# Optimization experiments

Measured on AMD Instinct MI355X. Metric: run time of the kernel, lower is better.

The kernel has to match this reference:

```python
import jax, jax.numpy as jnp
import numpy as np

NTAPS = 63
BATCH = 32
SAMPLES = 2_097_152


def setup_inputs() -> dict:
    key = jax.random.key(0)
    k1, k2, k3, k4 = jax.random.split(key, 4)
    x = jax.random.normal(k1, (BATCH, 1, SAMPLES), dtype=jnp.float32)
    b = jax.random.normal(k2, (BATCH, NTAPS), dtype=jnp.float32)
    # adaptor: torch.nn.Linear(63, 63) -> weight (out,in), bias (out,)
    W = jax.random.normal(k3, (NTAPS, NTAPS), dtype=jnp.float32) * (1.0 / np.sqrt(NTAPS))
    bias = jax.random.normal(k4, (NTAPS,), dtype=jnp.float32) * (1.0 / np.sqrt(NTAPS))
    return {"x": x, "b": b, "W": W, "bias": bias}


def reference(x, b, W, bias):
    # x: (bs, 1, s); b: (bs, ntaps)
    bs, ch, s = x.shape
    # adaptor: Linear on filter coefficients
    b = b @ W.T + bias                      # (bs, ntaps)
    ntaps = b.shape[-1]
    pad = ntaps // 2
    # same-length FIR (torch conv1d = cross-correlation)
    xp = jnp.pad(x, ((0, 0), (0, 0), (pad, pad)))   # (bs, 1, s + 2*pad)
    # batched per-sample filters via grouped conv: batch dim -> channel groups
    lhs = xp.reshape(1, bs * ch, -1)        # N=1, C=bs
    rhs = b.reshape(bs, 1, ntaps)           # O=bs, I=1, taps
    y = jax.lax.conv_general_dilated(
        lhs, rhs,
        window_strides=(1,),
        padding="VALID",
        dimension_numbers=("NCH", "OIH", "NCH"),
        feature_group_count=bs,
    )                                       # (1, bs, s)
    return y.reshape(bs, ch, s)
```

## Files before the change

kernel.cpp:

```cpp
#include <hip/hip_runtime.h>

#define NTAPS   63
#define NBATCH  32
#define SAMPLES 2097152
#define ROUT    16
#define BLOCK   256
#define CHUNK   (ROUT * BLOCK)
#define TILE_F  (CHUNK + 64)
#define TILE_B  (TILE_F / 4)
#define PSLOT(o) ((o) + ((o) >> 2))
#define LDS_B   (PSLOT(TILE_B - 1) + 1)

__global__ void filt_kernel(const float* __restrict__ b,
                            const float* __restrict__ W,
                            const float* __restrict__ bias,
                            float* __restrict__ filt) {
    const int batch = blockIdx.x;
    const int t = threadIdx.x;
    if (t < NTAPS) {
        const float* br = b + batch * NTAPS;
        const float* wr = W + t * NTAPS;
        float s = bias[t];
#pragma unroll
        for (int k = 0; k < NTAPS; ++k) s = fmaf(br[k], wr[k], s);
        filt[batch * NTAPS + t] = s;
    }
}

__global__ __launch_bounds__(BLOCK) void fir_kernel(const float* __restrict__ x,
                                                    const float* __restrict__ filt,
                                                    float* __restrict__ y) {
    __shared__ float4 tile[LDS_B];

    const int tid = threadIdx.x;
    const int batch = blockIdx.y;
    const int chunk0 = blockIdx.x * CHUNK;
    const float* __restrict__ xb = x + (size_t)batch * SAMPLES;
    float*       __restrict__ yb = y + (size_t)batch * SAMPLES;
    const float* __restrict__ bf = filt + batch * NTAPS;

    const bool interior = (blockIdx.x != 0) && (blockIdx.x != gridDim.x - 1);
    if (interior) {
#pragma unroll
        for (int r = 0; r < 4; ++r) {
            const int o = r * BLOCK + tid;
            const float4 v = *reinterpret_cast<const float4*>(xb + chunk0 - 32 + 4 * o);
            tile[PSLOT(o)] = v;
        }
        if (tid < TILE_B - 4 * BLOCK) {
            const int o = 4 * BLOCK + tid;
            const float4 v = *reinterpret_cast<const float4*>(xb + chunk0 - 32 + 4 * o);
            tile[PSLOT(o)] = v;
        }
    } else {
#pragma unroll
        for (int r = 0; r < 5; ++r) {
            const int o = r * BLOCK + tid;
            if (o < TILE_B) {
                const int gi = chunk0 - 32 + 4 * o;
                float4 v;
                v.x = (gi + 0 >= 0 && gi + 0 < SAMPLES) ? xb[gi + 0] : 0.0f;
                v.y = (gi + 1 >= 0 && gi + 1 < SAMPLES) ? xb[gi + 1] : 0.0f;
                v.z = (gi + 2 >= 0 && gi + 2 < SAMPLES) ? xb[gi + 2] : 0.0f;
                v.w = (gi + 3 >= 0 && gi + 3 < SAMPLES) ? xb[gi + 3] : 0.0f;
                tile[PSLOT(o)] = v;
            }
        }
    }
    __syncthreads();

    float w[80];
#pragma unroll
    for (int j = 0; j < 20; ++j) {
        const float4 v = tile[5 * tid + j + (j >> 2)];
        w[4 * j + 0] = v.x;
        w[4 * j + 1] = v.y;
        w[4 * j + 2] = v.z;
        w[4 * j + 3] = v.w;
    }

    float acc[ROUT];
#pragma unroll
    for (int r = 0; r < ROUT; ++r) acc[r] = 0.0f;

#pragma unroll
    for (int t = 0; t < NTAPS; ++t) {
        const float c = bf[t];
#pragma unroll
        for (int r = 0; r < ROUT; ++r) acc[r] = fmaf(c, w[r + t + 1], acc[r]);
    }

    const int s0 = chunk0 + tid * ROUT;
#pragma unroll
    for (int j = 0; j < ROUT / 4; ++j) {
        float4 v;
        v.x = acc[4 * j + 0];
        v.y = acc[4 * j + 1];
        v.z = acc[4 * j + 2];
        v.w = acc[4 * j + 3];
        *reinterpret_cast<float4*>(yb + s0 + 4 * j) = v;
    }
}

extern "C" void kernel_launch(void* const* d_in, const int* in_sizes, int n_in,
                              void* d_out, int out_size, void* d_ws, size_t ws_size,
                              hipStream_t stream) {
    const float* x    = (const float*)d_in[0];
    const float* b    = (const float*)d_in[1];
    const float* W    = (const float*)d_in[2];
    const float* bias = (const float*)d_in[3];
    float* y = (float*)d_out;
    float* filt = (float*)d_ws;

    filt_kernel<<<dim3(NBATCH), dim3(64), 0, stream>>>(b, W, bias, filt);

    dim3 grid(SAMPLES / CHUNK, NBATCH);
    fir_kernel<<<grid, dim3(BLOCK), 0, stream>>>(x, filt, y);
}
```

Baseline: 448.8 us.

## Make FIR blocks persistent over chunks with double-buffered LDS and register prefetch

Each block now processes eight consecutive chunks instead of one. The next chunk's input is prefetched into registers while the current chunk is computed, and is staged into a second LDS buffer between iterations. The goal is to hide global load latency behind the FMA work and to amortise block launch and filter-coefficient loads. In exchange, LDS use doubles and register pressure rises, which may lower occupancy, and the grid shrinks by a factor of eight.

```diff
diff --git a/kernel.cpp b/kernel.cpp
--- a/kernel.cpp
+++ b/kernel.cpp
@@ -6,10 +6,14 @@
 #define ROUT    16
 #define BLOCK   256
 #define CHUNK   (ROUT * BLOCK)
+#define NCHUNKS (SAMPLES / CHUNK)
+#define ITERS   8
+#define NBLKX   (NCHUNKS / ITERS)
 #define TILE_F  (CHUNK + 64)
 #define TILE_B  (TILE_F / 4)
 #define PSLOT(o) ((o) + ((o) >> 2))
 #define LDS_B   (PSLOT(TILE_B - 1) + 1)
+#define TAIL_B  (TILE_B - 4 * BLOCK)
 
 __global__ void filt_kernel(const float* __restrict__ b,
                             const float* __restrict__ W,
@@ -30,75 +34,99 @@
 __global__ __launch_bounds__(BLOCK) void fir_kernel(const float* __restrict__ x,
                                                     const float* __restrict__ filt,
                                                     float* __restrict__ y) {
-    __shared__ float4 tile[LDS_B];
+    __shared__ float4 tileA[LDS_B];
+    __shared__ float4 tileB[LDS_B];
 
-    const int tid = threadIdx.x;
+    const int tid   = threadIdx.x;
     const int batch = blockIdx.y;
-    const int chunk0 = blockIdx.x * CHUNK;
+    const int c0    = blockIdx.x * ITERS;
     const float* __restrict__ xb = x + (size_t)batch * SAMPLES;
     float*       __restrict__ yb = y + (size_t)batch * SAMPLES;
     const float* __restrict__ bf = filt + batch * NTAPS;
 
-    const bool interior = (blockIdx.x != 0) && (blockIdx.x != gridDim.x - 1);
-    if (interior) {
+    float4 p0, p1, p2, p3, p4;
+
+    auto load_tile = [&](int c) {
+        const int base = c * CHUNK - 32;
+        if (c != 0 && c != NCHUNKS - 1) {
+            p0 = *reinterpret_cast<const float4*>(xb + base + 4 * (0 * BLOCK + tid));
+            p1 = *reinterpret_cast<const float4*>(xb + base + 4 * (1 * BLOCK + tid));
+            p2 = *reinterpret_cast<const float4*>(xb + base + 4 * (2 * BLOCK + tid));
+            p3 = *reinterpret_cast<const float4*>(xb + base + 4 * (3 * BLOCK + tid));
+            if (tid < TAIL_B)
+                p4 = *reinterpret_cast<const float4*>(xb + base + 4 * (4 * BLOCK + tid));
+        } else {
+            float4* pr[5] = {&p0, &p1, &p2, &p3, &p4};
 #pragma unroll
-        for (int r = 0; r < 4; ++r) {
-            const int o = r * BLOCK + tid;
-            const float4 v = *reinterpret_cast<const float4*>(xb + chunk0 - 32 + 4 * o);
-            tile[PSLOT(o)] = v;
-        }
-        if (tid < TILE_B - 4 * BLOCK) {
-            const int o = 4 * BLOCK + tid;
-            const float4 v = *reinterpret_cast<const float4*>(xb + chunk0 - 32 + 4 * o);
-            tile[PSLOT(o)] = v;
-        }
-    } else {
-#pragma unroll
-        for (int r = 0; r < 5; ++r) {
-            const int o = r * BLOCK + tid;
-            if (o < TILE_B) {
-                const int gi = chunk0 - 32 + 4 * o;
-                float4 v;
-                v.x = (gi + 0 >= 0 && gi + 0 < SAMPLES) ? xb[gi + 0] : 0.0f;
-                v.y = (gi + 1 >= 0 && gi + 1 < SAMPLES) ? xb[gi + 1] : 0.0f;
-                v.z = (gi + 2 >= 0 && gi + 2 < SAMPLES) ? xb[gi + 2] : 0.0f;
-                v.w = (gi + 3 >= 0 && gi + 3 < SAMPLES) ? xb[gi + 3] : 0.0f;
-                tile[PSLOT(o)] = v;
+            for (int r = 0; r < 5; ++r) {
+                const int o = r * BLOCK + tid;
+                if (o < TILE_B) {
+                    const int gi = base + 4 * o;
+                    float4 v;
+                    v.x = (gi + 0 >= 0 && gi + 0 < SAMPLES) ? xb[gi + 0] : 0.0f;
+                    v.y = (gi + 1 >= 0 && gi + 1 < SAMPLES) ? xb[gi + 1] : 0.0f;
+                    v.z = (gi + 2 >= 0 && gi + 2 < SAMPLES) ? xb[gi + 2] : 0.0f;
+                    v.w = (gi + 3 >= 0 && gi + 3 < SAMPLES) ? xb[gi + 3] : 0.0f;
+                    *pr[r] = v;
+                }
             }
         }
-    }
-    __syncthreads();
+    };
 
-    float w[80];
+    auto store_tile = [&](float4* dst) {
+        dst[PSLOT(0 * BLOCK + tid)] = p0;
+        dst[PSLOT(1 * BLOCK + tid)] = p1;
+        dst[PSLOT(2 * BLOCK + tid)] = p2;
+        dst[PSLOT(3 * BLOCK + tid)] = p3;
+        if (tid < TAIL_B) dst[PSLOT(4 * BLOCK + tid)] = p4;
+    };
+
+    load_tile(c0);
+    store_tile(tileA);
+    load_tile(c0 + 1);
+    asm volatile("s_waitcnt lgkmcnt(0)" ::: "memory");
+    __builtin_amdgcn_s_barrier();
+
+    float4* curT = tileA;
+    float4* nxtT = tileB;
+
+    for (int it = 0; it < ITERS; ++it) {
+        float w[80];
 #pragma unroll
-    for (int j = 0; j < 20; ++j) {
-        const float4 v = tile[5 * tid + j + (j >> 2)];
-        w[4 * j + 0] = v.x;
-        w[4 * j + 1] = v.y;
-        w[4 * j + 2] = v.z;
-        w[4 * j + 3] = v.w;
-    }
+        for (int j = 0; j < 20; ++j) {
+            const float4 v = curT[5 * tid + j + (j >> 2)];
+            w[4 * j + 0] = v.x;
+            w[4 * j + 1] = v.y;
+            w[4 * j + 2] = v.z;
+            w[4 * j + 3] = v.w;
+        }
+        float acc[ROUT];
+#pragma unroll
+        for (int r = 0; r < ROUT; ++r) acc[r] = 0.0f;
+#pragma unroll
+        for (int t = 0; t < NTAPS; ++t) {
+            const float c = bf[t];
+#pragma unroll
+            for (int r = 0; r < ROUT; ++r) acc[r] = fmaf(c, w[r + t + 1], acc[r]);
+        }
+        const int s0 = (c0 + it) * CHUNK + tid * ROUT;
+#pragma unroll
+        for (int j = 0; j < 4; ++j) {
+            float4 v;
+            v.x = acc[4 * j + 0];
+            v.y = acc[4 * j + 1];
+            v.z = acc[4 * j + 2];
+            v.w = acc[4 * j + 3];
+            *reinterpret_cast<float4*>(yb + s0 + 4 * j) = v;
+        }
 
-    float acc[ROUT];
-#pragma unroll
-    for (int r = 0; r < ROUT; ++r) acc[r] = 0.0f;
-
-#pragma unroll
-    for (int t = 0; t < NTAPS; ++t) {
-        const float c = bf[t];
-#pragma unroll
-        for (int r = 0; r < ROUT; ++r) acc[r] = fmaf(c, w[r + t + 1], acc[r]);
-    }
-
-    const int s0 = chunk0 + tid * ROUT;
-#pragma unroll
-    for (int j = 0; j < ROUT / 4; ++j) {
-        float4 v;
-        v.x = acc[4 * j + 0];
-        v.y = acc[4 * j + 1];
-        v.z = acc[4 * j + 2];
-        v.w = acc[4 * j + 3];
-        *reinterpret_cast<float4*>(yb + s0 + 4 * j) = v;
+        if (it < ITERS - 1) {
+            store_tile(nxtT);
+            if (it < ITERS - 2) load_tile(c0 + it + 2);
+            asm volatile("s_waitcnt lgkmcnt(0)" ::: "memory");
+            __builtin_amdgcn_s_barrier();
+            float4* tmp = curT; curT = nxtT; nxtT = tmp;
+        }
     }
 }
 
@@ -114,6 +142,6 @@
 
     filt_kernel<<<dim3(NBATCH), dim3(64), 0, stream>>>(b, W, bias, filt);
 
-    dim3 grid(SAMPLES / CHUNK, NBATCH);
+    dim3 grid(NBLKX, NBATCH);
     fir_kernel<<<grid, dim3(BLOCK), 0, stream>>>(x, filt, y);
 }
```

New measurement: 482.7 us. 7.6% more time.
